# Kernel optimization log

Measured on AMD Instinct MI355X. Metric: run time of the kernel, lower is better.

## Reference

```python
import jax, jax.numpy as jnp
import numpy as np

B, N, M, F = 4, 2048, 100, 42   # batch, natoms, max_neighbors, nFeatures
H1, H2 = 64, 32                 # hidden sizes (nNodes), output size 1


def setup_inputs() -> dict:
    key = jax.random.key(0)
    ks = jax.random.split(key, 12)
    image = jax.random.normal(ks[0], (B, N, F), jnp.float32)
    dfeat = jax.random.normal(ks[1], (B, N, M, F, 3), jnp.float32) * 0.1
    # 1-based neighbor indices; 0 would mean "no neighbor" (all valid here)
    neighbor = jax.random.randint(ks[2], (B, N, M), 1, N + 1).astype(jnp.int64)
    Egroup_weight = jax.random.uniform(ks[3], (B, N, N), dtype=jnp.float32)
    divider = jnp.ones((B, N, 1), jnp.float32)
    W0 = jax.random.normal(ks[4], (H1, F), jnp.float32) * 0.1
    b0 = jax.random.normal(ks[5], (H1,), jnp.float32) * 0.1
    W1 = jax.random.normal(ks[6], (H2, H1), jnp.float32) * 0.1
    b1 = jax.random.normal(ks[7], (H2,), jnp.float32) * 0.1
    W2 = jax.random.normal(ks[8], (1, H2), jnp.float32) * 0.1
    b2 = jax.random.normal(ks[9], (1,), jnp.float32) * 0.1
    return dict(image=image, dfeat=dfeat, Egroup_weight=Egroup_weight,
                divider=divider, W0=W0, b0=b0, W1=W1, b1=b1, W2=W2, b2=b2,
                neighbor=neighbor)


def reference(image, dfeat, Egroup_weight, divider, W0, b0, W1, b1, W2, b2, neighbor):
    # --- per-atom MLP (FCNet): ACTIVE = softplus, dACTIVE = sigmoid ---
    z0 = image @ W0.T + b0            # [B,N,H1]
    L0 = jax.nn.softplus(z0)
    d0 = jax.nn.sigmoid(z0)
    z1 = L0 @ W1.T + b1               # [B,N,H2]
    L1 = jax.nn.softplus(z1)
    d1 = jax.nn.sigmoid(z1)
    Ei = L1 @ W2.T + b2               # [B,N,1] per-atom energy

    # --- analytic dEi/dx (the grad chain in FCNet, identical to autograd) ---
    g = d1 * W2                       # [B,N,H2]
    g = g @ W1                        # [B,N,H1]
    g = d0 * g
    dE = g @ W0                       # [B,N,F]

    Etot = Ei.sum(axis=1)             # [B,1]

    # --- force: gather neighbor dE rows, contract with dfeat, per-atom sum ---
    flag = (neighbor > 0).astype(dE.dtype)          # [B,N,M]
    idx = jnp.maximum(neighbor - 1, 0)              # 0-based, padded safe
    dE_nb = jax.vmap(lambda d, i: d[i])(dE, idx)    # [B,N,M,F] gather over atoms
    force = jnp.einsum('bnmf,bnmfc->bnc', dE_nb * flag[..., None], dfeat)  # [B,N,3]

    return Etot, Ei, force
```

## Files before the change

### kernel.cpp

```cpp
#include <hip/hip_runtime.h>
#include <hip/hip_bf16.h>
#include <math.h>

#define BATCH   4
#define NATOMS  2048
#define MNEIGH  100
#define NFEAT   42
#define H1      64
#define H2      32
#define NPAIR   (MNEIGH * NFEAT)
#define NGRP    (NPAIR / 4)
#define APB     8
#define GATH    17

__device__ __forceinline__ float softplus_f(float z) {
    if (z > 20.f) return z;
    return log1pf(expf(z));
}

__device__ __forceinline__ float sigmoid_f(float z) {
    return 1.f / (1.f + expf(-z));
}

__global__ __launch_bounds__(256) void mlp_kernel(
    const float* __restrict__ image,
    const float* __restrict__ W0, const float* __restrict__ b0,
    const float* __restrict__ W1, const float* __restrict__ b1,
    const float* __restrict__ W2, const float* __restrict__ b2,
    float* __restrict__ Ei_out,
    float* __restrict__ dE)
{
    __shared__ float sW0 [H1 * NFEAT];
    __shared__ float sW0T[NFEAT * H1];
    __shared__ float sW1 [H2 * H1];
    __shared__ float sW1T[H1 * H2];
    __shared__ float sW2[H2];
    __shared__ float sb0[H1];
    __shared__ float sb1[H2];

    const int tid = threadIdx.x;
    for (int i = tid; i < H1 * NFEAT; i += 256) {
        const float v = W0[i];
        sW0[i] = v;
        const int h = i / NFEAT, f = i - h * NFEAT;
        sW0T[f * H1 + h] = v;
    }
    for (int i = tid; i < H2 * H1; i += 256) {
        const float v = W1[i];
        sW1[i] = v;
        const int h2 = i >> 6, h = i & 63;
        sW1T[h * H2 + h2] = v;
    }
    if (tid < H2) { sW2[tid] = W2[tid]; sb1[tid] = b1[tid]; }
    if (tid < H1) sb0[tid] = b0[tid];
    const float bias2 = b2[0];
    __syncthreads();

    const int wave = tid >> 6;
    const int lane = tid & 63;
    const int l2   = lane & 31;
    const int lf   = (lane < NFEAT) ? lane : NFEAT - 1;
    const int ga0  = blockIdx.x * 16 + wave * 4;

    float img[4];
    #pragma unroll
    for (int a = 0; a < 4; ++a)
        img[a] = (lane < NFEAT) ? image[(size_t)(ga0 + a) * NFEAT + lane] : 0.f;

    float z0a[4], z0b[4];
    #pragma unroll
    for (int a = 0; a < 4; ++a) { z0a[a] = sb0[lane]; z0b[a] = 0.f; }
    #pragma unroll
    for (int f = 0; f < NFEAT; f += 2) {
        const float wA = sW0T[f * H1 + lane];
        const float wB = sW0T[(f + 1) * H1 + lane];
        #pragma unroll
        for (int a = 0; a < 4; ++a) {
            z0a[a] = fmaf(__shfl(img[a], f,     64), wA, z0a[a]);
            z0b[a] = fmaf(__shfl(img[a], f + 1, 64), wB, z0b[a]);
        }
    }
    float L0[4], d0[4];
    #pragma unroll
    for (int a = 0; a < 4; ++a) {
        const float z = z0a[a] + z0b[a];
        L0[a] = softplus_f(z);
        d0[a] = sigmoid_f(z);
    }

    float z1a[4], z1b[4];
    #pragma unroll
    for (int a = 0; a < 4; ++a) { z1a[a] = sb1[l2]; z1b[a] = 0.f; }
    #pragma unroll
    for (int h = 0; h < H1; h += 2) {
        const float wA = sW1T[h * H2 + l2];
        const float wB = sW1T[(h + 1) * H2 + l2];
        #pragma unroll
        for (int a = 0; a < 4; ++a) {
            z1a[a] = fmaf(__shfl(L0[a], h,     64), wA, z1a[a]);
            z1b[a] = fmaf(__shfl(L0[a], h + 1, 64), wB, z1b[a]);
        }
    }
    const float w2 = sW2[l2];
    float d1[4];
    #pragma unroll
    for (int a = 0; a < 4; ++a) {
        const float z = z1a[a] + z1b[a];
        const float L1 = softplus_f(z);
        d1[a] = sigmoid_f(z);
        float ei = (lane < H2) ? L1 * w2 : 0.f;
        #pragma unroll
        for (int off = 16; off > 0; off >>= 1) ei += __shfl_down(ei, off, 64);
        if (lane == 0) Ei_out[ga0 + a] = ei + bias2;
    }

    float g2v[4];
    #pragma unroll
    for (int a = 0; a < 4; ++a) g2v[a] = d1[a] * w2;
    float g1a[4], g1b[4];
    #pragma unroll
    for (int a = 0; a < 4; ++a) { g1a[a] = 0.f; g1b[a] = 0.f; }
    #pragma unroll
    for (int h2 = 0; h2 < H2; h2 += 2) {
        const float wA = sW1[h2 * H1 + lane];
        const float wB = sW1[(h2 + 1) * H1 + lane];
        #pragma unroll
        for (int a = 0; a < 4; ++a) {
            g1a[a] = fmaf(__shfl(g2v[a], h2,     64), wA, g1a[a]);
            g1b[a] = fmaf(__shfl(g2v[a], h2 + 1, 64), wB, g1b[a]);
        }
    }
    float g1[4];
    #pragma unroll
    for (int a = 0; a < 4; ++a) g1[a] = (g1a[a] + g1b[a]) * d0[a];

    float sa[4], sb[4];
    #pragma unroll
    for (int a = 0; a < 4; ++a) { sa[a] = 0.f; sb[a] = 0.f; }
    #pragma unroll
    for (int h = 0; h < H1; h += 2) {
        const float wA = sW0[h * NFEAT + lf];
        const float wB = sW0[(h + 1) * NFEAT + lf];
        #pragma unroll
        for (int a = 0; a < 4; ++a) {
            sa[a] = fmaf(__shfl(g1[a], h,     64), wA, sa[a]);
            sb[a] = fmaf(__shfl(g1[a], h + 1, 64), wB, sb[a]);
        }
    }
    if (lane < NFEAT) {
        #pragma unroll
        for (int a = 0; a < 4; ++a)
            dE[(size_t)(ga0 + a) * NFEAT + lane] = sa[a] + sb[a];
    }
}

__global__ __launch_bounds__(256) void etot_kernel(
    const float* __restrict__ Ei, float* __restrict__ Etot)
{
    const int b = blockIdx.x;
    const int tid = threadIdx.x;
    float s = 0.f;
    for (int n = tid; n < NATOMS; n += 256) s += Ei[(size_t)b * NATOMS + n];
    #pragma unroll
    for (int off = 32; off > 0; off >>= 1) s += __shfl_down(s, off, 64);
    __shared__ float rb[4];
    if ((tid & 63) == 0) rb[tid >> 6] = s;
    __syncthreads();
    if (tid == 0) Etot[b] = rb[0] + rb[1] + rb[2] + rb[3];
}

__global__ __launch_bounds__(256) void force_kernel(
    const float* __restrict__ dfeat,
    const int*   __restrict__ neighbor,
    const float* __restrict__ dE,
    float* __restrict__ force)
{
    __shared__ float sdE[2][NPAIR];
    __shared__ int   snbr[APB * MNEIGH];
    __shared__ float rbuf[4][3];

    const int tid     = threadIdx.x;
    const int ga0     = blockIdx.x * APB;
    const int rowbase = (ga0 >> 11) * NATOMS;
    const int wave    = tid >> 6, lane = tid & 63;

    for (int i = tid; i < APB * MNEIGH; i += 256)
        snbr[i] = neighbor[(size_t)ga0 * MNEIGH + i];
    __syncthreads();

    float gv[GATH];
    #pragma unroll
    for (int t = 0; t < GATH; ++t) {
        const int j = tid + 256 * t;
        float v = 0.f;
        if (j < NPAIR) {
            const int m  = j / NFEAT;
            const int f  = j - m * NFEAT;
            const int nb = snbr[m];
            const int row = rowbase + ((nb > 0) ? nb - 1 : 0);
            const float d = dE[(size_t)row * NFEAT + f];
            v = (nb > 0) ? d : 0.f;
        }
        gv[t] = v;
    }

    for (int k = 0; k < APB; ++k) {
        #pragma unroll
        for (int t = 0; t < GATH; ++t) {
            const int j = tid + 256 * t;
            if (j < NPAIR) sdE[k & 1][j] = gv[t];
        }
        __syncthreads();

        if (k + 1 < APB) {
            #pragma unroll
            for (int t = 0; t < GATH; ++t) {
                const int j = tid + 256 * t;
                float v = 0.f;
                if (j < NPAIR) {
                    const int m  = j / NFEAT;
                    const int f  = j - m * NFEAT;
                    const int nb = snbr[(k + 1) * MNEIGH + m];
                    const int row = rowbase + ((nb > 0) ? nb - 1 : 0);
                    const float d = dE[(size_t)row * NFEAT + f];
                    v = (nb > 0) ? d : 0.f;
                }
                gv[t] = v;
            }
        }

        const float4* __restrict__ dfb4 =
            (const float4*)(dfeat + (size_t)(ga0 + k) * (NPAIR * 3));
        const float4* __restrict__ s4 = (const float4*)sdE[k & 1];
        float a0 = 0.f, a1 = 0.f, a2 = 0.f;
        for (int g = tid; g < NGRP; g += 256) {
            const float4 w  = s4[g];
            const float4 v0 = dfb4[3 * g];
            const float4 v1 = dfb4[3 * g + 1];
            const float4 v2 = dfb4[3 * g + 2];
            a0 = fmaf(v0.x, w.x, a0); a1 = fmaf(v0.y, w.x, a1); a2 = fmaf(v0.z, w.x, a2);
            a0 = fmaf(v0.w, w.y, a0); a1 = fmaf(v1.x, w.y, a1); a2 = fmaf(v1.y, w.y, a2);
            a0 = fmaf(v1.z, w.z, a0); a1 = fmaf(v1.w, w.z, a1); a2 = fmaf(v2.x, w.z, a2);
            a0 = fmaf(v2.y, w.w, a0); a1 = fmaf(v2.z, w.w, a1); a2 = fmaf(v2.w, w.w, a2);
        }

        #pragma unroll
        for (int off = 32; off > 0; off >>= 1) {
            a0 += __shfl_down(a0, off, 64);
            a1 += __shfl_down(a1, off, 64);
            a2 += __shfl_down(a2, off, 64);
        }
        if (lane == 0) { rbuf[wave][0] = a0; rbuf[wave][1] = a1; rbuf[wave][2] = a2; }
        __syncthreads();
        if (tid < 3)
            force[(size_t)(ga0 + k) * 3 + tid] =
                rbuf[0][tid] + rbuf[1][tid] + rbuf[2][tid] + rbuf[3][tid];
    }
}

extern "C" void kernel_launch(void* const* d_in, const int* in_sizes, int n_in,
                              void* d_out, int out_size, void* d_ws, size_t ws_size,
                              hipStream_t stream) {
    const float* image = (const float*)d_in[0];
    const float* dfeat = (const float*)d_in[1];
    const float* W0 = (const float*)d_in[4];
    const float* b0 = (const float*)d_in[5];
    const float* W1 = (const float*)d_in[6];
    const float* b1 = (const float*)d_in[7];
    const float* W2 = (const float*)d_in[8];
    const float* b2 = (const float*)d_in[9];
    const int*   neighbor = (const int*)d_in[10];

    float* out   = (float*)d_out;
    float* Etot  = out;
    float* Ei    = out + BATCH;
    float* force = out + BATCH + BATCH * NATOMS;
    float* dE    = (float*)d_ws;

    mlp_kernel<<<BATCH * NATOMS / 16, 256, 0, stream>>>(
        image, W0, b0, W1, b1, W2, b2, Ei, dE);
    etot_kernel<<<BATCH, 256, 0, stream>>>(Ei, Etot);
    force_kernel<<<BATCH * NATOMS / APB, 256, 0, stream>>>(dfeat, neighbor, dE, force);
}
```

Measured before the change: 129.8 us.

## Assign one wave per atom in force kernel with direct global gathers

Rewrites the force kernel so each wavefront computes one atom's force independently. The shared-memory staging of gathered dE rows and the per-atom block barriers are removed, and neighbor dE values are read straight from global memory inside the dfeat streaming loop. This is meant to remove synchronization and staging overhead so the dfeat stream stays saturated. In exchange it issues about two gathered cache loads per float4 and adds index arithmetic to map flattened quads to pairs.

New measurement: 137.7 us. +6.1%, slower.

```diff
diff --git a/kernel.cpp b/kernel.cpp
--- a/kernel.cpp
+++ b/kernel.cpp
@@ -9,9 +9,7 @@
 #define H1      64
 #define H2      32
 #define NPAIR   (MNEIGH * NFEAT)
-#define NGRP    (NPAIR / 4)
-#define APB     8
-#define GATH    17
+#define NQUAD   (NPAIR * 3 / 4)
 
 __device__ __forceinline__ float softplus_f(float z) {
     if (z > 20.f) return z;
@@ -175,86 +173,59 @@
     const float* __restrict__ dE,
     float* __restrict__ force)
 {
-    __shared__ float sdE[2][NPAIR];
-    __shared__ int   snbr[APB * MNEIGH];
-    __shared__ float rbuf[4][3];
-
-    const int tid     = threadIdx.x;
-    const int ga0     = blockIdx.x * APB;
-    const int rowbase = (ga0 >> 11) * NATOMS;
-    const int wave    = tid >> 6, lane = tid & 63;
-
-    for (int i = tid; i < APB * MNEIGH; i += 256)
-        snbr[i] = neighbor[(size_t)ga0 * MNEIGH + i];
+    __shared__ int snbr[4 * MNEIGH];
+
+    const int tid  = threadIdx.x;
+    const int wave = tid >> 6, lane = tid & 63;
+    const int ga   = blockIdx.x * 4 + wave;
+    const int b    = ga >> 11;
+
+    for (int i = tid; i < 4 * MNEIGH; i += 256)
+        snbr[i] = neighbor[(size_t)(blockIdx.x * 4) * MNEIGH + i];
     __syncthreads();
 
-    float gv[GATH];
-    #pragma unroll
-    for (int t = 0; t < GATH; ++t) {
-        const int j = tid + 256 * t;
-        float v = 0.f;
-        if (j < NPAIR) {
-            const int m  = j / NFEAT;
-            const int f  = j - m * NFEAT;
-            const int nb = snbr[m];
-            const int row = rowbase + ((nb > 0) ? nb - 1 : 0);
-            const float d = dE[(size_t)row * NFEAT + f];
-            v = (nb > 0) ? d : 0.f;
-        }
-        gv[t] = v;
-    }
-
-    for (int k = 0; k < APB; ++k) {
-        #pragma unroll
-        for (int t = 0; t < GATH; ++t) {
-            const int j = tid + 256 * t;
-            if (j < NPAIR) sdE[k & 1][j] = gv[t];
-        }
-        __syncthreads();
-
-        if (k + 1 < APB) {
-            #pragma unroll
-            for (int t = 0; t < GATH; ++t) {
-                const int j = tid + 256 * t;
-                float v = 0.f;
-                if (j < NPAIR) {
-                    const int m  = j / NFEAT;
-                    const int f  = j - m * NFEAT;
-                    const int nb = snbr[(k + 1) * MNEIGH + m];
-                    const int row = rowbase + ((nb > 0) ? nb - 1 : 0);
-                    const float d = dE[(size_t)row * NFEAT + f];
-                    v = (nb > 0) ? d : 0.f;
-                }
-                gv[t] = v;
-            }
-        }
-
-        const float4* __restrict__ dfb4 =
-            (const float4*)(dfeat + (size_t)(ga0 + k) * (NPAIR * 3));
-        const float4* __restrict__ s4 = (const float4*)sdE[k & 1];
-        float a0 = 0.f, a1 = 0.f, a2 = 0.f;
-        for (int g = tid; g < NGRP; g += 256) {
-            const float4 w  = s4[g];
-            const float4 v0 = dfb4[3 * g];
-            const float4 v1 = dfb4[3 * g + 1];
-            const float4 v2 = dfb4[3 * g + 2];
-            a0 = fmaf(v0.x, w.x, a0); a1 = fmaf(v0.y, w.x, a1); a2 = fmaf(v0.z, w.x, a2);
-            a0 = fmaf(v0.w, w.y, a0); a1 = fmaf(v1.x, w.y, a1); a2 = fmaf(v1.y, w.y, a2);
-            a0 = fmaf(v1.z, w.z, a0); a1 = fmaf(v1.w, w.z, a1); a2 = fmaf(v2.x, w.z, a2);
-            a0 = fmaf(v2.y, w.w, a0); a1 = fmaf(v2.z, w.w, a1); a2 = fmaf(v2.w, w.w, a2);
-        }
-
-        #pragma unroll
-        for (int off = 32; off > 0; off >>= 1) {
-            a0 += __shfl_down(a0, off, 64);
-            a1 += __shfl_down(a1, off, 64);
-            a2 += __shfl_down(a2, off, 64);
-        }
-        if (lane == 0) { rbuf[wave][0] = a0; rbuf[wave][1] = a1; rbuf[wave][2] = a2; }
-        __syncthreads();
-        if (tid < 3)
-            force[(size_t)(ga0 + k) * 3 + tid] =
-                rbuf[0][tid] + rbuf[1][tid] + rbuf[2][tid] + rbuf[3][tid];
+    const int* __restrict__ nb = snbr + wave * MNEIGH;
+    const float* __restrict__ dErow = dE + (size_t)b * NATOMS * NFEAT;
+    const float4* __restrict__ dfb4 =
+        (const float4*)(dfeat + (size_t)ga * (NPAIR * 3));
+
+    float a0 = 0.f, a1 = 0.f, a2 = 0.f;
+    #pragma unroll 2
+    for (int i = 0; i < 50; ++i) {
+        const int q = lane + 64 * i;
+        if (q < NQUAD) {
+            const int i0 = 4 * q;
+            const int p0 = i0 / 3;
+            const int r0 = i0 - 3 * p0;
+            const int p1 = p0 + 1;
+            const int m0 = p0 / 42, f0 = p0 - 42 * m0;
+            const int m1 = p1 / 42, f1 = p1 - 42 * m1;
+            const int n0 = nb[m0], n1 = nb[m1];
+            const float w0r = dErow[(size_t)((n0 > 0 ? n0 - 1 : 0)) * NFEAT + f0];
+            const float w1r = dErow[(size_t)((n1 > 0 ? n1 - 1 : 0)) * NFEAT + f1];
+            const float w0 = (n0 > 0) ? w0r : 0.f;
+            const float w1 = (n1 > 0) ? w1r : 0.f;
+            const float4 v = dfb4[q];
+            const float s0 = fmaf(v.x, w0, v.w * w1);
+            const float s1 = v.y * ((r0 >= 2) ? w1 : w0);
+            const float s2 = v.z * ((r0 >= 1) ? w1 : w0);
+            const bool e0 = (r0 == 0), e1 = (r0 == 1);
+            a0 += e0 ? s0 : (e1 ? s2 : s1);
+            a1 += e0 ? s1 : (e1 ? s0 : s2);
+            a2 += e0 ? s2 : (e1 ? s1 : s0);
+        }
+    }
+
+    #pragma unroll
+    for (int off = 32; off > 0; off >>= 1) {
+        a0 += __shfl_down(a0, off, 64);
+        a1 += __shfl_down(a1, off, 64);
+        a2 += __shfl_down(a2, off, 64);
+    }
+    if (lane == 0) {
+        force[(size_t)ga * 3 + 0] = a0;
+        force[(size_t)ga * 3 + 1] = a1;
+        force[(size_t)ga * 3 + 2] = a2;
     }
 }
 
@@ -280,5 +251,5 @@
     mlp_kernel<<<BATCH * NATOMS / 16, 256, 0, stream>>>(
         image, W0, b0, W1, b1, W2, b2, Ei, dE);
     etot_kernel<<<BATCH, 256, 0, stream>>>(Ei, Etot);
-    force_kernel<<<BATCH * NATOMS / APB, 256, 0, stream>>>(dfeat, neighbor, dE, force);
-}
+    force_kernel<<<BATCH * NATOMS / 4, 256, 0, stream>>>(dfeat, neighbor, dE, force);
+}
```

## Rewrite MLP kernel as one thread per atom with scalar weight loads

Applied to the files above, without the earlier changes.

Replaces the wave-cooperative MLP, which used shuffles and shared-memory weight copies with four atoms per wave, with a one-thread-per-atom design. Each thread keeps its features and accumulators in registers and reads the weights as uniform scalar loads. The first layer is recomputed in the backward pass instead of storing per-hidden activations. This removes the shared-memory staging and the shuffle traffic, but it launches only 128 single-wave blocks, uses many registers, and gives uncoalesced strided image loads and dE stores.

Result: slower. 220.1 us (+69.6%).

```diff
diff --git a/kernel.cpp b/kernel.cpp
--- a/kernel.cpp
+++ b/kernel.cpp
@@ -22,7 +22,7 @@
     return 1.f / (1.f + expf(-z));
 }
 
-__global__ __launch_bounds__(256) void mlp_kernel(
+__global__ __launch_bounds__(64) void mlp_kernel(
     const float* __restrict__ image,
     const float* __restrict__ W0, const float* __restrict__ b0,
     const float* __restrict__ W1, const float* __restrict__ b1,
@@ -30,128 +30,69 @@
     float* __restrict__ Ei_out,
     float* __restrict__ dE)
 {
-    __shared__ float sW0 [H1 * NFEAT];
-    __shared__ float sW0T[NFEAT * H1];
-    __shared__ float sW1 [H2 * H1];
-    __shared__ float sW1T[H1 * H2];
-    __shared__ float sW2[H2];
-    __shared__ float sb0[H1];
-    __shared__ float sb1[H2];
-
-    const int tid = threadIdx.x;
-    for (int i = tid; i < H1 * NFEAT; i += 256) {
-        const float v = W0[i];
-        sW0[i] = v;
-        const int h = i / NFEAT, f = i - h * NFEAT;
-        sW0T[f * H1 + h] = v;
-    }
-    for (int i = tid; i < H2 * H1; i += 256) {
-        const float v = W1[i];
-        sW1[i] = v;
-        const int h2 = i >> 6, h = i & 63;
-        sW1T[h * H2 + h2] = v;
-    }
-    if (tid < H2) { sW2[tid] = W2[tid]; sb1[tid] = b1[tid]; }
-    if (tid < H1) sb0[tid] = b0[tid];
-    const float bias2 = b2[0];
-    __syncthreads();
-
-    const int wave = tid >> 6;
-    const int lane = tid & 63;
-    const int l2   = lane & 31;
-    const int lf   = (lane < NFEAT) ? lane : NFEAT - 1;
-    const int ga0  = blockIdx.x * 16 + wave * 4;
-
-    float img[4];
-    #pragma unroll
-    for (int a = 0; a < 4; ++a)
-        img[a] = (lane < NFEAT) ? image[(size_t)(ga0 + a) * NFEAT + lane] : 0.f;
-
-    float z0a[4], z0b[4];
-    #pragma unroll
-    for (int a = 0; a < 4; ++a) { z0a[a] = sb0[lane]; z0b[a] = 0.f; }
-    #pragma unroll
-    for (int f = 0; f < NFEAT; f += 2) {
-        const float wA = sW0T[f * H1 + lane];
-        const float wB = sW0T[(f + 1) * H1 + lane];
-        #pragma unroll
-        for (int a = 0; a < 4; ++a) {
-            z0a[a] = fmaf(__shfl(img[a], f,     64), wA, z0a[a]);
-            z0b[a] = fmaf(__shfl(img[a], f + 1, 64), wB, z0b[a]);
-        }
-    }
-    float L0[4], d0[4];
-    #pragma unroll
-    for (int a = 0; a < 4; ++a) {
-        const float z = z0a[a] + z0b[a];
-        L0[a] = softplus_f(z);
-        d0[a] = sigmoid_f(z);
-    }
-
-    float z1a[4], z1b[4];
-    #pragma unroll
-    for (int a = 0; a < 4; ++a) { z1a[a] = sb1[l2]; z1b[a] = 0.f; }
-    #pragma unroll
-    for (int h = 0; h < H1; h += 2) {
-        const float wA = sW1T[h * H2 + l2];
-        const float wB = sW1T[(h + 1) * H2 + l2];
-        #pragma unroll
-        for (int a = 0; a < 4; ++a) {
-            z1a[a] = fmaf(__shfl(L0[a], h,     64), wA, z1a[a]);
-            z1b[a] = fmaf(__shfl(L0[a], h + 1, 64), wB, z1b[a]);
-        }
-    }
-    const float w2 = sW2[l2];
-    float d1[4];
-    #pragma unroll
-    for (int a = 0; a < 4; ++a) {
-        const float z = z1a[a] + z1b[a];
-        const float L1 = softplus_f(z);
-        d1[a] = sigmoid_f(z);
-        float ei = (lane < H2) ? L1 * w2 : 0.f;
-        #pragma unroll
-        for (int off = 16; off > 0; off >>= 1) ei += __shfl_down(ei, off, 64);
-        if (lane == 0) Ei_out[ga0 + a] = ei + bias2;
-    }
-
-    float g2v[4];
-    #pragma unroll
-    for (int a = 0; a < 4; ++a) g2v[a] = d1[a] * w2;
-    float g1a[4], g1b[4];
-    #pragma unroll
-    for (int a = 0; a < 4; ++a) { g1a[a] = 0.f; g1b[a] = 0.f; }
-    #pragma unroll
-    for (int h2 = 0; h2 < H2; h2 += 2) {
-        const float wA = sW1[h2 * H1 + lane];
-        const float wB = sW1[(h2 + 1) * H1 + lane];
-        #pragma unroll
-        for (int a = 0; a < 4; ++a) {
-            g1a[a] = fmaf(__shfl(g2v[a], h2,     64), wA, g1a[a]);
-            g1b[a] = fmaf(__shfl(g2v[a], h2 + 1, 64), wB, g1b[a]);
-        }
-    }
-    float g1[4];
-    #pragma unroll
-    for (int a = 0; a < 4; ++a) g1[a] = (g1a[a] + g1b[a]) * d0[a];
-
-    float sa[4], sb[4];
-    #pragma unroll
-    for (int a = 0; a < 4; ++a) { sa[a] = 0.f; sb[a] = 0.f; }
-    #pragma unroll
-    for (int h = 0; h < H1; h += 2) {
-        const float wA = sW0[h * NFEAT + lf];
-        const float wB = sW0[(h + 1) * NFEAT + lf];
-        #pragma unroll
-        for (int a = 0; a < 4; ++a) {
-            sa[a] = fmaf(__shfl(g1[a], h,     64), wA, sa[a]);
-            sb[a] = fmaf(__shfl(g1[a], h + 1, 64), wB, sb[a]);
-        }
-    }
-    if (lane < NFEAT) {
-        #pragma unroll
-        for (int a = 0; a < 4; ++a)
-            dE[(size_t)(ga0 + a) * NFEAT + lane] = sa[a] + sb[a];
-    }
+    const int ga = blockIdx.x * 64 + threadIdx.x;
+
+    float img[NFEAT];
+    #pragma unroll
+    for (int f = 0; f < NFEAT; ++f)
+        img[f] = image[(size_t)ga * NFEAT + f];
+
+    float z1[H2];
+    #pragma unroll
+    for (int j = 0; j < H2; ++j) z1[j] = b1[j];
+
+    for (int h = 0; h < H1; ++h) {
+        float za = b0[h], zb = 0.f, zc = 0.f;
+        #pragma unroll
+        for (int f = 0; f < NFEAT; f += 3) {
+            za = fmaf(img[f],     W0[h * NFEAT + f],     za);
+            zb = fmaf(img[f + 1], W0[h * NFEAT + f + 1], zb);
+            zc = fmaf(img[f + 2], W0[h * NFEAT + f + 2], zc);
+        }
+        const float L0 = softplus_f(za + zb + zc);
+        #pragma unroll
+        for (int j = 0; j < H2; ++j)
+            z1[j] = fmaf(L0, W1[j * H1 + h], z1[j]);
+    }
+
+    float ei = b2[0];
+    float g2[H2];
+    #pragma unroll
+    for (int j = 0; j < H2; ++j) {
+        const float w2 = W2[j];
+        ei = fmaf(softplus_f(z1[j]), w2, ei);
+        g2[j] = sigmoid_f(z1[j]) * w2;
+    }
+    Ei_out[ga] = ei;
+
+    float dEa[NFEAT];
+    #pragma unroll
+    for (int f = 0; f < NFEAT; ++f) dEa[f] = 0.f;
+
+    for (int h = 0; h < H1; ++h) {
+        float za = b0[h], zb = 0.f, zc = 0.f;
+        #pragma unroll
+        for (int f = 0; f < NFEAT; f += 3) {
+            za = fmaf(img[f],     W0[h * NFEAT + f],     za);
+            zb = fmaf(img[f + 1], W0[h * NFEAT + f + 1], zb);
+            zc = fmaf(img[f + 2], W0[h * NFEAT + f + 2], zc);
+        }
+        const float d0 = sigmoid_f(za + zb + zc);
+        float gA = 0.f, gB = 0.f;
+        #pragma unroll
+        for (int j = 0; j < H2; j += 2) {
+            gA = fmaf(g2[j],     W1[j * H1 + h],       gA);
+            gB = fmaf(g2[j + 1], W1[(j + 1) * H1 + h], gB);
+        }
+        const float gh = (gA + gB) * d0;
+        #pragma unroll
+        for (int f = 0; f < NFEAT; ++f)
+            dEa[f] = fmaf(gh, W0[h * NFEAT + f], dEa[f]);
+    }
+
+    #pragma unroll
+    for (int f = 0; f < NFEAT; ++f)
+        dE[(size_t)ga * NFEAT + f] = dEa[f];
 }
 
 __global__ __launch_bounds__(256) void etot_kernel(
@@ -277,7 +218,7 @@
     float* force = out + BATCH + BATCH * NATOMS;
     float* dE    = (float*)d_ws;
 
-    mlp_kernel<<<BATCH * NATOMS / 16, 256, 0, stream>>>(
+    mlp_kernel<<<BATCH * NATOMS / 64, 64, 0, stream>>>(
         image, W0, b0, W1, b1, W2, b2, Ei, dE);
     etot_kernel<<<BATCH, 256, 0, stream>>>(Ei, Etot);
     force_kernel<<<BATCH * NATOMS / APB, 256, 0, stream>>>(dfeat, neighbor, dE, force);
```
